# Performance work log

Hardware: AMD Instinct MI355X
Metric: run time of the kernel (lower is better)

## Reference

```python
import jax, jax.numpy as jnp
import numpy as np

N = 20000      # num clique nodes
E = 320000     # num edges
H = 256        # hidden_channels
OUT = 128      # out_channels
T = 3          # num_timesteps
NEG = 0.01     # GAT negative_slope
NA = 60000     # num atoms (unused arg sizing)


def setup_inputs() -> dict:
    key = jax.random.key(0)
    ks = jax.random.split(key, 12)
    s = 1.0 / np.sqrt(H)
    return {
        "x_clique": jax.random.normal(ks[0], (N, H), jnp.float32),
        "W_gat": jax.random.normal(ks[1], (H, H), jnp.float32) * s,
        "att_src": jax.random.normal(ks[2], (H,), jnp.float32) * s,
        "att_dst": jax.random.normal(ks[3], (H,), jnp.float32) * s,
        "gat_bias": jnp.zeros((H,), jnp.float32),
        "W_ih": jax.random.normal(ks[4], (3 * H, H), jnp.float32) * s,
        "W_hh": jax.random.normal(ks[5], (3 * H, H), jnp.float32) * s,
        "b_ih": jnp.zeros((3 * H,), jnp.float32),
        "b_hh": jnp.zeros((3 * H,), jnp.float32),
        "lin_W": jax.random.normal(ks[6], (OUT, H), jnp.float32) * s,
        "lin_b": jnp.zeros((OUT,), jnp.float32),
        "atom2clique_index": jax.random.randint(ks[7], (2, NA), 0, N, jnp.int64),
        "mol_batch": jax.random.randint(ks[8], (NA,), 0, 32, jnp.int64),
        "clique_batch": jax.random.randint(ks[9], (N,), 0, 32, jnp.int64),
        "clique_edge_index": jax.random.randint(ks[10], (2, E), 0, N, jnp.int64),
    }


def _gat_conv(h, W_gat, att_src, att_dst, gat_bias, src, dst):
    # PyG GATConv, heads=1, no self loops. h: [N,H]
    xp = h @ W_gat.T                                   # [N,H]
    a_e = jax.nn.leaky_relu((xp @ att_src)[src] + (xp @ att_dst)[dst], NEG)  # [E]
    # segment softmax over destination nodes
    m = jax.ops.segment_max(a_e, dst, num_segments=N)  # [N] (-inf for empty)
    e = jnp.exp(a_e - m[dst])                          # [E]
    denom = jax.ops.segment_sum(e, dst, num_segments=N)
    coef = e / jnp.maximum(denom[dst], 1e-16)          # [E]
    out = jax.ops.segment_sum(coef[:, None] * xp[src], dst, num_segments=N)
    return out + gat_bias


def _gru_cell(x, h, W_ih, W_hh, b_ih, b_hh):
    gx = x @ W_ih.T + b_ih                             # [N,3H]
    gh = h @ W_hh.T + b_hh                             # [N,3H]
    xr, xz, xn = jnp.split(gx, 3, axis=-1)
    hr, hz, hn = jnp.split(gh, 3, axis=-1)
    r = jax.nn.sigmoid(xr + hr)
    z = jax.nn.sigmoid(xz + hz)
    n = jnp.tanh(xn + r * hn)
    return (1.0 - z) * n + z * h


def reference(x_clique, W_gat, att_src, att_dst, gat_bias, W_ih, W_hh, b_ih, b_hh,
              lin_W, lin_b, atom2clique_index, mol_batch, clique_batch,
              clique_edge_index):
    src = clique_edge_index[0]
    dst = clique_edge_index[1]
    h = x_clique
    for _ in range(T):  # fixed, small timestep count
        m = _gat_conv(h, W_gat, att_src, att_dst, gat_bias, src, dst)
        m = jax.nn.elu(m)  # dropout p=0.0 -> identity
        h = _gru_cell(m, h, W_ih, W_hh, b_ih, b_hh)
    return h @ lin_W.T + lin_b  # [N, OUT]
```

## Files before the change

kernel.cpp:

```cpp
#include <hip/hip_runtime.h>
#include <math.h>

#define NNODES 20000
#define NROWP  20096
#define NEDGES 320000
#define HDIM   256
#define ODIM   128
#define TSTEPS 3
#define KCAT   512

typedef __bf16 bf16x8 __attribute__((ext_vector_type(8)));
typedef __bf16 bf16x4 __attribute__((ext_vector_type(4)));
typedef float  f32x4  __attribute__((ext_vector_type(4)));

#define LOG2E 1.44269504f
__device__ __forceinline__ float fexp2_(float x){ return __builtin_amdgcn_exp2f(x); }
__device__ __forceinline__ float frcp_(float x){ return __builtin_amdgcn_rcpf(x); }
__device__ __forceinline__ float fsig_(float x){ return frcp_(1.f + fexp2_(-LOG2E*x)); }
__device__ __forceinline__ float ftanh_(float x){ float t = fexp2_(2.f*LOG2E*x); return 1.f - 2.f*frcp_(t+1.f); }
__device__ __forceinline__ float felu_(float x){ return (x>0.f)? x : (fexp2_(LOG2E*x)-1.f); }

__device__ __forceinline__ void load_lds16(const void* g, void* l){
  __builtin_amdgcn_global_load_lds((const __attribute__((address_space(1))) void*)g,
                                   (__attribute__((address_space(3))) void*)l, 16, 0, 0);
}

__device__ __forceinline__ bf16x8 lds_frag64(const __bf16* Ls, int rowbase, int lane, int kk){
  int row = rowbase + (lane&15);
  int g = (lane>>4) + (kk<<2);
  int slot = (row<<3) + (g ^ (row&7));
  return *(const bf16x8*)&Ls[slot<<3];
}

template<int NWG>
__device__ __forceinline__ int xcd_swz(int b){
  constexpr int Q = NWG/8, R = NWG%8;
  int x = b & 7, i = b >> 3;
  if (R == 0) return x*Q + i;
  return (x < R) ? (x*(Q+1) + i) : (R*(Q+1) + (x-R)*Q + i);
}

__global__ void setup1_kernel(const int* __restrict__ dst, int* __restrict__ deg,
                              const float* __restrict__ xc, __bf16* __restrict__ Acat,
                              const float* __restrict__ Wih, const float* __restrict__ Whh,
                              const float* __restrict__ Wg, const float* __restrict__ Lw,
                              __bf16* __restrict__ Bf, __bf16* __restrict__ wgb,
                              __bf16* __restrict__ lwb, float* __restrict__ asad){
  int i = blockIdx.x*blockDim.x + threadIdx.x;
  if (i < NEDGES) atomicAdd(&deg[dst[i]], 1);
  if (i < NNODES*64){
    int row = i>>6, c = (i&63)<<2;
    float4 v = *(const float4*)&xc[(size_t)row*HDIM + c];
    bf16x4 o; o[0]=(__bf16)v.x; o[1]=(__bf16)v.y; o[2]=(__bf16)v.z; o[3]=(__bf16)v.w;
    *(bf16x4*)&Acat[(size_t)row*KCAT + 256 + c] = o;
  }
  if (i < 1024*128){
    int row = i>>7, kc = (i&127)<<2;
    int gate = row>>8, c = row&255;
    float4 v = make_float4(0,0,0,0);
    if (gate==0 || gate==1){
      v = (kc<256) ? *(const float4*)&Wih[(size_t)(gate*256+c)*HDIM + kc]
                   : *(const float4*)&Whh[(size_t)(gate*256+c)*HDIM + kc-256];
    } else if (gate==2){
      if (kc<256) v = *(const float4*)&Wih[(size_t)(512+c)*HDIM + kc];
    } else {
      if (kc>=256) v = *(const float4*)&Whh[(size_t)(512+c)*HDIM + kc-256];
    }
    bf16x4 o; o[0]=(__bf16)v.x; o[1]=(__bf16)v.y; o[2]=(__bf16)v.z; o[3]=(__bf16)v.w;
    *(bf16x4*)&Bf[(size_t)row*KCAT + kc] = o;
  } else if (i < 1024*128 + 256*64){
    int j = i - 1024*128;
    float4 v = ((const float4*)Wg)[j];
    bf16x4 o; o[0]=(__bf16)v.x; o[1]=(__bf16)v.y; o[2]=(__bf16)v.z; o[3]=(__bf16)v.w;
    ((bf16x4*)wgb)[j] = o;
  } else if (i < 1024*128 + 256*64 + 128*64){
    int j = i - 1024*128 - 256*64;
    float4 v = ((const float4*)Lw)[j];
    bf16x4 o; o[0]=(__bf16)v.x; o[1]=(__bf16)v.y; o[2]=(__bf16)v.z; o[3]=(__bf16)v.w;
    ((bf16x4*)lwb)[j] = o;
  }
  if (i < 2*NNODES) asad[i] = 0.f;
}

__global__ void scan_kernel(const int* __restrict__ deg, int* __restrict__ rowptr){
  const int PER = 20;
  int tid = threadIdx.x, lane = tid&63, w = tid>>6;
  int base = tid*PER;
  int v[PER]; int s = 0;
  #pragma unroll
  for (int k=0;k<PER;k++){
    v[k] = (base+k < NNODES)? deg[base+k] : 0;
    s += v[k];
  }
  int incl = s;
  #pragma unroll
  for (int off=1; off<64; off<<=1){
    int t = __shfl_up(incl, off);
    if (lane >= off) incl += t;
  }
  __shared__ int wtot[16];
  if (lane==63) wtot[w] = incl;
  __syncthreads();
  if (w==0 && lane<16){
    int x = wtot[lane];
    #pragma unroll
    for (int off=1; off<16; off<<=1){
      int t = __shfl_up(x, off);
      if (lane >= off) x += t;
    }
    wtot[lane] = x;
  }
  __syncthreads();
  int wbase = (w>0)? wtot[w-1] : 0;
  int run = wbase + incl - s;
  #pragma unroll
  for (int k=0;k<PER;k++){
    if (base+k < NNODES) rowptr[base+k] = run;
    run += v[k];
  }
  if (tid==1023) rowptr[NNODES] = wbase + incl;
}

__global__ void scatter_kernel(const int* __restrict__ src, const int* __restrict__ dst,
                               const int* __restrict__ rowptr, int* __restrict__ fill,
                               int* __restrict__ ssrc){
  int e = blockIdx.x*blockDim.x + threadIdx.x;
  if (e < NEDGES){
    int d = dst[e];
    int pos = rowptr[d] + atomicAdd(&fill[d], 1);
    ssrc[pos] = src[e];
  }
}

template<int YC, bool F32OUT, bool ALPHA, int NWG>
__global__ __launch_bounds__(256,3)
void mfma_gemm_sm(const __bf16* __restrict__ A, int lda,
                  const __bf16* __restrict__ B,
                  const float* __restrict__ bias,
                  __bf16* __restrict__ Cb, float* __restrict__ Cf,
                  int ldc, int Mreal,
                  const float* __restrict__ att_s, const float* __restrict__ att_d,
                  float* __restrict__ as_, float* __restrict__ ad_){
  __shared__ __bf16 As[2][64*64];
  __shared__ __bf16 Bs[2][128*64];
  int wgid = xcd_swz<NWG>(blockIdx.x);
  int r0 = (wgid/YC)*64, c0 = (wgid%YC)*128;
  int tx = threadIdx.x, lane = tx&63, w = tx>>6;
  int rbase = (w&1)*32, cbase = (w>>1)*64;
  f32x4 acc[2][4] = {};

  auto stage = [&](int k0, int s){
    #pragma unroll
    for (int q=0;q<2;q++){
      int idx = q*256 + w*64 + lane;
      int row = idx>>3, kg = (idx&7) ^ (row&7);
      load_lds16(A + (size_t)(r0+row)*lda + k0 + (kg<<3),
                 (char*)&As[s][0] + (q*256 + w*64)*16);
    }
    #pragma unroll
    for (int q=0;q<4;q++){
      int idx = q*256 + w*64 + lane;
      int row = idx>>3, kg = (idx&7) ^ (row&7);
      load_lds16(B + (size_t)(c0+row)*HDIM + k0 + (kg<<3),
                 (char*)&Bs[s][0] + (q*256 + w*64)*16);
    }
  };

  stage(0, 0);
  __syncthreads();
  #pragma unroll
  for (int t=0; t<HDIM/64; t++){
    const int cur = t & 1;
    if (t+1 < HDIM/64) stage((t+1)*64, cur^1);
    #pragma unroll
    for (int kk=0;kk<2;kk++){
      bf16x8 a[2], bb[4];
      #pragma unroll
      for (int i=0;i<2;i++) a[i] = lds_frag64(&As[cur][0], rbase + i*16, lane, kk);
      #pragma unroll
      for (int j=0;j<4;j++) bb[j] = lds_frag64(&Bs[cur][0], cbase + j*16, lane, kk);
      #pragma unroll
      for (int i=0;i<2;i++)
        #pragma unroll
        for (int j=0;j<4;j++)
          acc[i][j] = __builtin_amdgcn_mfma_f32_16x16x32_bf16(a[i], bb[j], acc[i][j], 0,0,0);
    }
    __syncthreads();
  }
  int grb = r0 + rbase, gcb = c0 + cbase;
  #pragma unroll
  for (int i=0;i<2;i++){
    #pragma unroll
    for (int j=0;j<4;j++){
      int gc = gcb + j*16 + (lane&15);
      float bv = F32OUT ? bias[gc] : 0.f;
      #pragma unroll
      for (int r=0;r<4;r++){
        int gr = grb + i*16 + ((lane>>4)<<2) + r;
        if (gr >= Mreal) continue;
        float v = acc[i][j][r] + bv;
        if (F32OUT) Cf[(size_t)gr*ldc + gc] = v;
        else        Cb[(size_t)gr*ldc + gc] = (__bf16)v;
      }
    }
  }
  if (ALPHA){
    float ps[2][4] = {}, pd[2][4] = {};
    #pragma unroll
    for (int j=0;j<4;j++){
      int gc = gcb + j*16 + (lane&15);
      float sv = att_s[gc], dv = att_d[gc];
      #pragma unroll
      for (int i=0;i<2;i++)
        #pragma unroll
        for (int r=0;r<4;r++){
          ps[i][r] += acc[i][j][r]*sv;
          pd[i][r] += acc[i][j][r]*dv;
        }
    }
    #pragma unroll
    for (int m=1;m<16;m<<=1){
      #pragma unroll
      for (int i=0;i<2;i++)
        #pragma unroll
        for (int r=0;r<4;r++){
          ps[i][r] += __shfl_xor(ps[i][r], m);
          pd[i][r] += __shfl_xor(pd[i][r], m);
        }
    }
    if ((lane&15)==0){
      #pragma unroll
      for (int i=0;i<2;i++)
        #pragma unroll
        for (int r=0;r<4;r++){
          int gr = grb + i*16 + ((lane>>4)<<2) + r;
          if (gr < Mreal){
            atomicAdd(&as_[gr], ps[i][r]);
            atomicAdd(&ad_[gr], pd[i][r]);
          }
        }
    }
  }
}

__global__ __launch_bounds__(256,8)
void gat_aggregate_kernel(const __bf16* __restrict__ xpb, const float* __restrict__ as_,
                          const float* __restrict__ ad_, const int* __restrict__ rowptr,
                          const int* __restrict__ ssrc, const float* __restrict__ gat_bias,
                          __bf16* __restrict__ Acat){
  int node = blockIdx.x*4 + (threadIdx.x>>6);
  int lane = threadIdx.x & 63;
  if (node >= NNODES) return;
  int beg = rowptr[node], end = rowptr[node+1];
  int deg = end - beg;
  float adv = ad_[node];
  int half = lane>>5, col = lane&31;

  float acc[8] = {0,0,0,0,0,0,0,0};

  if (deg <= 64){
    float a = -INFINITY; int sreg = 0;
    if (lane < deg){
      sreg = ssrc[beg+lane];
      a = as_[sreg] + adv;
      a = (a>0.f)? a : 0.01f*a;
    }
    float mx = a;
    #pragma unroll
    for (int off=32; off; off>>=1) mx = fmaxf(mx, __shfl_xor(mx,off));
    float e = (lane<deg)? fexp2_(LOG2E*(a-mx)) : 0.f;
    float sm = e;
    #pragma unroll
    for (int off=32; off; off>>=1) sm += __shfl_xor(sm,off);
    float creg = e*frcp_(fmaxf(sm,1e-16f));

    int j = 0;
    for (; j+16<=deg; j+=16){
      float cc[8]; int rr[8]; bf16x8 vv[8];
      #pragma unroll
      for (int k=0;k<8;k++){
        cc[k] = __shfl(creg, j+2*k+half);
        rr[k] = __shfl(sreg, j+2*k+half);
      }
      #pragma unroll
      for (int k=0;k<8;k++) vv[k] = *(const bf16x8*)&xpb[(size_t)rr[k]*HDIM + col*8];
      #pragma unroll
      for (int k=0;k<8;k++)
        #pragma unroll
        for (int t=0;t<8;t++) acc[t] += cc[k]*(float)vv[k][t];
    }
    for (; j+8<=deg; j+=8){
      float cc[4]; int rr[4]; bf16x8 vv[4];
      #pragma unroll
      for (int k=0;k<4;k++){
        cc[k] = __shfl(creg, j+2*k+half);
        rr[k] = __shfl(sreg, j+2*k+half);
      }
      #pragma unroll
      for (int k=0;k<4;k++) vv[k] = *(const bf16x8*)&xpb[(size_t)rr[k]*HDIM + col*8];
      #pragma unroll
      for (int k=0;k<4;k++)
        #pragma unroll
        for (int t=0;t<8;t++) acc[t] += cc[k]*(float)vv[k][t];
    }
    for (; j+4<=deg; j+=4){
      float c0=__shfl(creg,j+half),  c1=__shfl(creg,j+2+half);
      int   r0=__shfl(sreg,j+half),  r1=__shfl(sreg,j+2+half);
      bf16x8 v0 = *(const bf16x8*)&xpb[(size_t)r0*HDIM + col*8];
      bf16x8 v1 = *(const bf16x8*)&xpb[(size_t)r1*HDIM + col*8];
      #pragma unroll
      for (int t=0;t<8;t++) acc[t] += c0*(float)v0[t] + c1*(float)v1[t];
    }
    for (; j<deg; j+=2){
      int jj = j + half;
      float cf = __shfl(creg, jj);
      int   rw = __shfl(sreg, jj);
      if (jj < deg){
        bf16x8 v = *(const bf16x8*)&xpb[(size_t)rw*HDIM + col*8];
        #pragma unroll
        for (int t=0;t<8;t++) acc[t] += cf*(float)v[t];
      }
    }
  } else {
    float mx = -INFINITY;
    for (int e=beg+lane; e<end; e+=64){
      float a = as_[ssrc[e]] + adv;
      a = (a>0.f)? a : 0.01f*a;
      mx = fmaxf(mx, a);
    }
    #pragma unroll
    for (int off=32; off; off>>=1) mx = fmaxf(mx, __shfl_xor(mx,off));
    float sm = 0.f;
    for (int e=beg+lane; e<end; e+=64){
      float a = as_[ssrc[e]] + adv;
      a = (a>0.f)? a : 0.01f*a;
      sm += fexp2_(LOG2E*(a-mx));
    }
    #pragma unroll
    for (int off=32; off; off>>=1) sm += __shfl_xor(sm,off);
    float rsc = frcp_(fmaxf(sm,1e-16f));
    for (int j=0; j<deg; j+=2){
      int jj = j + half;
      if (jj < deg){
        int rw = ssrc[beg+jj];
        float a = as_[rw] + adv;
        a = (a>0.f)? a : 0.01f*a;
        float cf = fexp2_(LOG2E*(a-mx))*rsc;
        bf16x8 v = *(const bf16x8*)&xpb[(size_t)rw*HDIM + col*8];
        #pragma unroll
        for (int t=0;t<8;t++) acc[t] += cf*(float)v[t];
      }
    }
  }

  #pragma unroll
  for (int t=0;t<8;t++) acc[t] += __shfl_down(acc[t], 32);
  if (half==0){
    float4 b0 = *(const float4*)&gat_bias[col*8];
    float4 b1 = *(const float4*)&gat_bias[col*8+4];
    float bb[8] = {b0.x,b0.y,b0.z,b0.w,b1.x,b1.y,b1.z,b1.w};
    bf16x8 ov;
    #pragma unroll
    for (int t=0;t<8;t++) ov[t] = (__bf16)felu_(acc[t]+bb[t]);
    *(bf16x8*)&Acat[(size_t)node*KCAT + col*8] = ov;
  }
}

#define RB128 (NROWP/128)
__global__ __launch_bounds__(256,2)
void gru_mfma_kernel(const __bf16* __restrict__ Acat, __bf16* __restrict__ AcatN,
                     const __bf16* __restrict__ Bf,
                     const float* __restrict__ bih, const float* __restrict__ bhh,
                     float* __restrict__ as_, float* __restrict__ ad_){
  __shared__ __bf16 As[2][128*64];
  __shared__ __bf16 Bs[2][128*64];
  int wgid = xcd_swz<RB128*8>(blockIdx.x);
  int r0 = (wgid>>3)*128, c0 = (wgid&7)*32;
  int tx = threadIdx.x, lane = tx&63, w = tx>>6;
  int rbase = w*32;
  f32x4 acc[4][2][2] = {};

  auto stage = [&](int k0, int s){
    #pragma unroll
    for (int q=0;q<4;q++){
      int idx = q*256 + w*64 + lane;
      int row = idx>>3, kg = (idx&7) ^ (row&7);
      load_lds16(Acat + (size_t)(r0+row)*KCAT + k0 + (kg<<3),
                 (char*)&As[s][0] + (q*256 + w*64)*16);
    }
    #pragma unroll
    for (int q=0;q<4;q++){
      int idx = q*256 + w*64 + lane;
      int row = idx>>3, kg = (idx&7) ^ (row&7);
      int gate = row>>5, colr = row&31;
      load_lds16(Bf + (size_t)(gate*256 + c0 + colr)*KCAT + k0 + (kg<<3),
                 (char*)&Bs[s][0] + (q*256 + w*64)*16);
    }
  };

  stage(0, 0);
  __syncthreads();
  #pragma unroll
  for (int t=0; t<KCAT/64; t++){
    const int cur = t & 1;
    if (t+1 < KCAT/64) stage((t+1)*64, cur^1);
    #pragma unroll
    for (int kk=0;kk<2;kk++){
      bf16x8 a[2], bb[4][2];
      #pragma unroll
      for (int i=0;i<2;i++) a[i] = lds_frag64(&As[cur][0], rbase + i*16, lane, kk);
      #pragma unroll
      for (int g=0;g<4;g++)
        #pragma unroll
        for (int j=0;j<2;j++) bb[g][j] = lds_frag64(&Bs[cur][0], g*32 + j*16, lane, kk);
      #pragma unroll
      for (int g=0;g<4;g++)
        #pragma unroll
        for (int i=0;i<2;i++)
          #pragma unroll
          for (int j=0;j<2;j++)
            acc[g][i][j] = __builtin_amdgcn_mfma_f32_16x16x32_bf16(a[i], bb[g][j], acc[g][i][j], 0,0,0);
    }
    __syncthreads();
  }
  int grb = r0 + rbase;
  #pragma unroll
  for (int i=0;i<2;i++){
    #pragma unroll
    for (int j=0;j<2;j++){
      int gc = c0 + j*16 + (lane&15);
      float br_ = bih[gc]     + bhh[gc];
      float bz_ = bih[256+gc] + bhh[256+gc];
      float bnx = bih[512+gc];
      float bnh = bhh[512+gc];
      #pragma unroll
      for (int r=0;r<4;r++){
        int gr = grb + i*16 + ((lane>>4)<<2) + r;
        if (gr >= NNODES) continue;
        float hold = (float)Acat[(size_t)gr*KCAT + 256 + gc];
        float rr = fsig_(acc[0][i][j][r] + br_);
        float zz = fsig_(acc[1][i][j][r] + bz_);
        float nn = ftanh_(acc[2][i][j][r] + bnx + rr*(acc[3][i][j][r] + bnh));
        AcatN[(size_t)gr*KCAT + 256 + gc] = (__bf16)((1.f-zz)*nn + zz*hold);
      }
    }
  }
  if ((wgid&7)==0 && (lane&15)==0){
    #pragma unroll
    for (int i=0;i<2;i++)
      #pragma unroll
      for (int r=0;r<4;r++){
        int gr = grb + i*16 + ((lane>>4)<<2) + r;
        if (gr < NNODES){ as_[gr] = 0.f; ad_[gr] = 0.f; }
      }
  }
}

extern "C" void kernel_launch(void* const* d_in, const int* in_sizes, int n_in,
                              void* d_out, int out_size, void* d_ws, size_t ws_size,
                              hipStream_t stream) {
  const float* x_clique = (const float*)d_in[0];
  const float* W_gat    = (const float*)d_in[1];
  const float* att_src  = (const float*)d_in[2];
  const float* att_dst  = (const float*)d_in[3];
  const float* gat_bias = (const float*)d_in[4];
  const float* W_ih     = (const float*)d_in[5];
  const float* W_hh     = (const float*)d_in[6];
  const float* b_ih     = (const float*)d_in[7];
  const float* b_hh     = (const float*)d_in[8];
  const float* lin_W    = (const float*)d_in[9];
  const float* lin_b    = (const float*)d_in[10];
  const int*   eidx     = (const int*)d_in[14];
  float* out = (float*)d_out;

  const int* src = eidx;
  const int* dst = eidx + NEDGES;

  const size_t ACAT = (size_t)NROWP*KCAT;
  __bf16* AcA  = (__bf16*)d_ws;
  __bf16* AcB  = AcA + ACAT;
  __bf16* xpb  = AcB + ACAT;
  __bf16* Bf   = xpb + (size_t)NROWP*HDIM;
  __bf16* wgb  = Bf  + (size_t)1024*KCAT;
  __bf16* lwb  = wgb + (size_t)HDIM*HDIM;
  float* as_   = (float*)(lwb + (size_t)ODIM*HDIM);
  float* ad_   = as_ + NNODES;
  int* deg     = (int*)(ad_ + NNODES);
  int* fill    = deg + NNODES;
  int* rowptr  = fill + NNODES;
  int* ssrc    = rowptr + (NNODES+1);

  hipMemsetAsync(deg, 0, 2*NNODES*sizeof(int), stream);
  setup1_kernel<<<NNODES*64/256, 256, 0, stream>>>(
      dst, deg, x_clique, AcA, W_ih, W_hh, W_gat, lin_W, Bf, wgb, lwb, as_);
  scan_kernel<<<1, 1024, 0, stream>>>(deg, rowptr);
  scatter_kernel<<<(NEDGES+255)/256, 256, 0, stream>>>(src, dst, rowptr, fill, ssrc);

  const int RB64 = NROWP/64;
  __bf16* Ac = AcA;
  __bf16* An = AcB;
  for (int t=0; t<TSTEPS; t++){
    mfma_gemm_sm<2,false,true,(NROWP/64)*2><<<RB64*2, 256, 0, stream>>>(
        Ac + 256, KCAT, wgb, nullptr, xpb, nullptr, HDIM, NNODES,
        att_src, att_dst, as_, ad_);
    gat_aggregate_kernel<<<(NNODES+3)/4, 256, 0, stream>>>(xpb, as_, ad_, rowptr, ssrc, gat_bias, Ac);
    gru_mfma_kernel<<<RB128*8, 256, 0, stream>>>(Ac, An, Bf, b_ih, b_hh, as_, ad_);
    __bf16* tmp = Ac; Ac = An; An = tmp;
  }
  mfma_gemm_sm<1,true,false,NROWP/64><<<RB64, 256, 0, stream>>>(
      Ac + 256, KCAT, lwb, lin_b, nullptr, out, ODIM, NNODES,
      nullptr, nullptr, nullptr, nullptr);
}
```

Before: 368.3 us.

## Skip zero GRU gate blocks and single-buffer GAT GEMM for occupancy

The GRU GEMM concatenates [m, h] along K against a fused weight. The separate xn and hn gates only need their own half of K (the other half of the fused weight is presumably zero). The kernel now loads and multiplies only three 32-column B tiles per K step, choosing the n-gate row by K half, which cuts a quarter of MFMA work and B traffic. Separately, the projection GEMM drops LDS double buffering and raises launch_bounds occupancy from 3 to 4, trading load/compute overlap for more resident waves.

```diff
diff --git a/kernel.cpp b/kernel.cpp
--- a/kernel.cpp
+++ b/kernel.cpp
@@ -133,7 +133,7 @@
 }
 
 template<int YC, bool F32OUT, bool ALPHA, int NWG>
-__global__ __launch_bounds__(256,3)
+__global__ __launch_bounds__(256,4)
 void mfma_gemm_sm(const __bf16* __restrict__ A, int lda,
                   const __bf16* __restrict__ B,
                   const float* __restrict__ bias,
@@ -141,44 +141,36 @@
                   int ldc, int Mreal,
                   const float* __restrict__ att_s, const float* __restrict__ att_d,
                   float* __restrict__ as_, float* __restrict__ ad_){
-  __shared__ __bf16 As[2][64*64];
-  __shared__ __bf16 Bs[2][128*64];
+  __shared__ __bf16 As[64*64];
+  __shared__ __bf16 Bs[128*64];
   int wgid = xcd_swz<NWG>(blockIdx.x);
   int r0 = (wgid/YC)*64, c0 = (wgid%YC)*128;
   int tx = threadIdx.x, lane = tx&63, w = tx>>6;
   int rbase = (w&1)*32, cbase = (w>>1)*64;
   f32x4 acc[2][4] = {};
-
-  auto stage = [&](int k0, int s){
+  for (int k0=0; k0<HDIM; k0+=64){
     #pragma unroll
     for (int q=0;q<2;q++){
       int idx = q*256 + w*64 + lane;
       int row = idx>>3, kg = (idx&7) ^ (row&7);
       load_lds16(A + (size_t)(r0+row)*lda + k0 + (kg<<3),
-                 (char*)&As[s][0] + (q*256 + w*64)*16);
+                 (char*)As + (q*256 + w*64)*16);
     }
     #pragma unroll
     for (int q=0;q<4;q++){
       int idx = q*256 + w*64 + lane;
       int row = idx>>3, kg = (idx&7) ^ (row&7);
       load_lds16(B + (size_t)(c0+row)*HDIM + k0 + (kg<<3),
-                 (char*)&Bs[s][0] + (q*256 + w*64)*16);
-    }
-  };
-
-  stage(0, 0);
-  __syncthreads();
-  #pragma unroll
-  for (int t=0; t<HDIM/64; t++){
-    const int cur = t & 1;
-    if (t+1 < HDIM/64) stage((t+1)*64, cur^1);
+                 (char*)Bs + (q*256 + w*64)*16);
+    }
+    __syncthreads();
     #pragma unroll
     for (int kk=0;kk<2;kk++){
       bf16x8 a[2], bb[4];
       #pragma unroll
-      for (int i=0;i<2;i++) a[i] = lds_frag64(&As[cur][0], rbase + i*16, lane, kk);
-      #pragma unroll
-      for (int j=0;j<4;j++) bb[j] = lds_frag64(&Bs[cur][0], cbase + j*16, lane, kk);
+      for (int i=0;i<2;i++) a[i] = lds_frag64(As, rbase + i*16, lane, kk);
+      #pragma unroll
+      for (int j=0;j<4;j++) bb[j] = lds_frag64(Bs, cbase + j*16, lane, kk);
       #pragma unroll
       for (int i=0;i<2;i++)
         #pragma unroll
@@ -373,14 +365,14 @@
                      const float* __restrict__ bih, const float* __restrict__ bhh,
                      float* __restrict__ as_, float* __restrict__ ad_){
   __shared__ __bf16 As[2][128*64];
-  __shared__ __bf16 Bs[2][128*64];
+  __shared__ __bf16 Bs[2][96*64];
   int wgid = xcd_swz<RB128*8>(blockIdx.x);
   int r0 = (wgid>>3)*128, c0 = (wgid&7)*32;
   int tx = threadIdx.x, lane = tx&63, w = tx>>6;
   int rbase = w*32;
   f32x4 acc[4][2][2] = {};
 
-  auto stage = [&](int k0, int s){
+  auto stage = [&](int k0, int s, int tg){
     #pragma unroll
     for (int q=0;q<4;q++){
       int idx = q*256 + w*64 + lane;
@@ -389,37 +381,44 @@
                  (char*)&As[s][0] + (q*256 + w*64)*16);
     }
     #pragma unroll
-    for (int q=0;q<4;q++){
+    for (int q=0;q<3;q++){
       int idx = q*256 + w*64 + lane;
       int row = idx>>3, kg = (idx&7) ^ (row&7);
-      int gate = row>>5, colr = row&31;
-      load_lds16(Bf + (size_t)(gate*256 + c0 + colr)*KCAT + k0 + (kg<<3),
+      int gsel = row>>5;
+      int grow = (gsel==2 ? tg : gsel)*256 + c0 + (row&31);
+      load_lds16(Bf + (size_t)grow*KCAT + k0 + (kg<<3),
                  (char*)&Bs[s][0] + (q*256 + w*64)*16);
     }
   };
 
-  stage(0, 0);
+  stage(0, 0, 2);
   __syncthreads();
   #pragma unroll
   for (int t=0; t<KCAT/64; t++){
     const int cur = t & 1;
-    if (t+1 < KCAT/64) stage((t+1)*64, cur^1);
+    if (t+1 < KCAT/64) stage((t+1)*64, cur^1, (t+1<4)?2:3);
     #pragma unroll
     for (int kk=0;kk<2;kk++){
-      bf16x8 a[2], bb[4][2];
+      bf16x8 a[2], b0[2], b1[2], bt[2];
       #pragma unroll
       for (int i=0;i<2;i++) a[i] = lds_frag64(&As[cur][0], rbase + i*16, lane, kk);
       #pragma unroll
-      for (int g=0;g<4;g++)
-        #pragma unroll
-        for (int j=0;j<2;j++) bb[g][j] = lds_frag64(&Bs[cur][0], g*32 + j*16, lane, kk);
-      #pragma unroll
-      for (int g=0;g<4;g++)
-        #pragma unroll
-        for (int i=0;i<2;i++)
-          #pragma unroll
-          for (int j=0;j<2;j++)
-            acc[g][i][j] = __builtin_amdgcn_mfma_f32_16x16x32_bf16(a[i], bb[g][j], acc[g][i][j], 0,0,0);
+      for (int j=0;j<2;j++){
+        b0[j] = lds_frag64(&Bs[cur][0], 0  + j*16, lane, kk);
+        b1[j] = lds_frag64(&Bs[cur][0], 32 + j*16, lane, kk);
+        bt[j] = lds_frag64(&Bs[cur][0], 64 + j*16, lane, kk);
+      }
+      #pragma unroll
+      for (int i=0;i<2;i++)
+        #pragma unroll
+        for (int j=0;j<2;j++){
+          acc[0][i][j] = __builtin_amdgcn_mfma_f32_16x16x32_bf16(a[i], b0[j], acc[0][i][j], 0,0,0);
+          acc[1][i][j] = __builtin_amdgcn_mfma_f32_16x16x32_bf16(a[i], b1[j], acc[1][i][j], 0,0,0);
+          if (t < 4)
+            acc[2][i][j] = __builtin_amdgcn_mfma_f32_16x16x32_bf16(a[i], bt[j], acc[2][i][j], 0,0,0);
+          else
+            acc[3][i][j] = __builtin_amdgcn_mfma_f32_16x16x32_bf16(a[i], bt[j], acc[3][i][j], 0,0,0);
+        }
     }
     __syncthreads();
   }
```

After: 356.2 us. 3.3% less time.
